# Kernel optimization log

Hardware: AMD Instinct MI355X
Metric: run time of the kernel (lower is better)

The kernel has to match this reference:

```python
import jax, jax.numpy as jnp
import numpy as np

# heavy-atom counts minus 1 (the residue_len) for the 20 standard amino acids
# GLY ALA SER CYS THR VAL PRO LEU ILE ASN ASP MET GLN GLU LYS HIS PHE ARG TYR TRP
NATOMS = np.array([4,5,6,6,7,7,7,8,8,8,8,8,9,9,9,10,11,11,12,14], dtype=np.int64)
NTYPES = 20
MAXA = int(NATOMS.max())  # 14
B, R, VDIM, NLIN = 128, 512, 256, 3


def setup_inputs() -> dict:
    rng = np.random.default_rng(0)
    type_ids = rng.integers(0, NTYPES, size=R)                     # metadata.seq as type ids
    natoms = NATOMS[type_ids]                                      # per-residue atom count
    residue_indices = np.concatenate([[0], np.cumsum(natoms)[:-1]])  # start atom of each residue
    n_atoms = int(natoms.sum())

    key = jax.random.key(0)
    k1, k2, k3 = jax.random.split(key, 3)
    x = jax.random.normal(k1, (B, n_atoms, 3), dtype=jnp.float32)

    # per-type first-layer weight, zero-padded beyond each type's natom so the
    # padded gathered atoms contribute exactly zero (identical math to slicing)
    pad_mask = (np.arange(MAXA)[None, :] < NATOMS[:, None]).astype(np.float32)  # (T, A)
    W0 = jax.random.normal(k2, (NTYPES, VDIM, MAXA), dtype=jnp.float32)
    W0 = W0 * (1.0 / np.sqrt(MAXA)) * jnp.asarray(pad_mask)[:, None, :]
    Wh = jax.random.normal(k3, (NTYPES, NLIN - 1, VDIM, VDIM), dtype=jnp.float32) * (1.0 / np.sqrt(VDIM))

    return {
        "x": x,
        "W0": W0,
        "Wh": Wh,
        "type_ids": jnp.asarray(type_ids, dtype=jnp.int64),
        "residue_indices": jnp.asarray(residue_indices, dtype=jnp.int64),
    }


def reference(x, W0, Wh, type_ids, residue_indices):
    """x:(B, atoms, 3) -> pos_ca:(B, R, 3), x_v:(B, R, VDIM, 3)"""
    n_atoms = x.shape[1]
    # gather each residue's atom window, padded to MAXA (clip keeps indices in
    # range; padded entries are killed by the zero-padded W0 columns)
    atom_idx = jnp.clip(residue_indices[:, None] + jnp.arange(MAXA)[None, :], 0, n_atoms - 1)  # (R, A)
    gathered = x[:, atom_idx]                               # (B, R, A, 3)
    root = x[:, residue_indices + 1]                        # (B, R, 3)  -- CA atom (x[:,1] of each slice)
    delta = gathered - root[:, :, None, :]                  # subtract root

    h = jnp.einsum('rva,brac->brvc', W0[type_ids], delta)   # per-type VecLinear(natom -> vdim)
    for l in range(NLIN - 1):                               # per-type VecLinear(vdim -> vdim)
        h = jnp.einsum('rvu,bruc->brvc', Wh[type_ids, l], h)

    pos_ca = root                                            # x[:, residue_indices + 1]
    return pos_ca, h
```

## Files before the change

### kernel.cpp

```cpp
#include <hip/hip_runtime.h>

namespace {
constexpr int NB = 128;
constexpr int NR = 512;
constexpr int ND = 256;
constexpr int NA = 14;

using short8 = __attribute__((ext_vector_type(8))) short;
using f32x4  = __attribute__((ext_vector_type(4))) float;

constexpr size_t WH_US  = (size_t)40 * 16 * 8 * 64 * 8;
constexpr size_t W0_OFF = WH_US;
constexpr size_t W0_US  = (size_t)20 * 16 * 64 * 8;
constexpr size_t RMAP_BYTE_OFF = (WH_US + W0_US) * 2;
constexpr size_t WS_NEEDED = RMAP_BYTE_OFF + NR * sizeof(int);

__device__ __forceinline__ unsigned short f2bf(float f) {
    unsigned int u = __float_as_uint(f);
    u = (u + 0x7FFFu + ((u >> 16) & 1u)) >> 16;
    return (unsigned short)u;
}
__device__ __forceinline__ int vswz(int v) { return v ^ (((v >> 5) & 3) << 3); }
}

__global__ void conv_wh(const float* __restrict__ Wh, unsigned short* __restrict__ ws) {
    int g = blockIdx.x * 256 + threadIdx.x;
    if (g >= 40 * 16 * 8 * 64) return;
    const int lane = g & 63, kt = (g >> 6) & 7, mt = (g >> 9) & 15, tl = g >> 13;
    const int v = mt * 16 + (lane & 15);
    const int u0 = kt * 32 + (lane >> 4) * 8;
    const float* src = Wh + ((size_t)tl * ND + v) * ND + u0;
    unsigned short o[8];
#pragma unroll
    for (int j = 0; j < 8; ++j) o[j] = f2bf(src[j]);
    uint4 pk;
    pk.x = o[0] | ((unsigned)o[1] << 16); pk.y = o[2] | ((unsigned)o[3] << 16);
    pk.z = o[4] | ((unsigned)o[5] << 16); pk.w = o[6] | ((unsigned)o[7] << 16);
    *reinterpret_cast<uint4*>(ws + (size_t)g * 8) = pk;
}

__global__ void conv_w0(const float* __restrict__ W0, unsigned short* __restrict__ ws) {
    int g = blockIdx.x * 256 + threadIdx.x;
    if (g >= 20 * 16 * 64) return;
    const int lane = g & 63, mt = (g >> 6) & 15, t = g >> 10;
    const int v = mt * 16 + (lane & 15);
    const int a0 = (lane >> 4) * 8;
    unsigned short o[8];
#pragma unroll
    for (int j = 0; j < 8; ++j) {
        const int a = a0 + j;
        o[j] = (a < NA) ? f2bf(W0[((size_t)t * ND + v) * NA + a]) : (unsigned short)0;
    }
    uint4 pk;
    pk.x = o[0] | ((unsigned)o[1] << 16); pk.y = o[2] | ((unsigned)o[3] << 16);
    pk.z = o[4] | ((unsigned)o[5] << 16); pk.w = o[6] | ((unsigned)o[7] << 16);
    *reinterpret_cast<uint4*>(ws + W0_OFF + (size_t)g * 8) = pk;
}

__global__ void build_rmap(const int* __restrict__ type_ids, int* __restrict__ rmap) {
    __shared__ int tl[NR];
    const int tid = threadIdx.x;
    tl[tid] = type_ids[tid];
    __syncthreads();
    const int myt = tl[tid];
    int pos = 0;
    for (int j = 0; j < NR; ++j) {
        const int tj = tl[j];
        pos += (tj < myt) || (tj == myt && j < tid);
    }
    rmap[pos] = tid;
}

__global__ __launch_bounds__(512, 6) void residues_mfma(
    const float* __restrict__ x, const unsigned short* __restrict__ wsw,
    const int* __restrict__ rmap, const int* __restrict__ type_ids,
    const int* __restrict__ res_idx, float* __restrict__ out, int n_atoms)
{
    const int tid = threadIdx.x, lane = tid & 63, w = tid >> 6;
    const int xcd = blockIdx.x & 7, j = blockIdx.x >> 3;
    const int r = rmap[xcd * 64 + (j >> 3)];
    const int b0 = (j & 7) * 16;
    const int ri = res_idx[r], t = type_ids[r];

    __shared__ __align__(16) unsigned short HT[48 * 264];
    __shared__ __align__(16) float fstc[24 * 260];
    unsigned short* dltT = HT;

    const unsigned short* w0b = wsw + W0_OFF + (size_t)t * (16 * 64 * 8);
    short8 a0[2];
#pragma unroll
    for (int mi = 0; mi < 2; ++mi)
        a0[mi] = *reinterpret_cast<const short8*>(w0b + (((w * 2 + mi) * 64) + lane) * 8);

    {
        const int bl = tid >> 5, k = tid & 31;
        const float* xb = x + (size_t)(b0 + bl) * n_atoms * 3;
        if (k < 16) {
            int atom = ri + k; if (atom > n_atoms - 1) atom = n_atoms - 1;
            const float* src  = xb + (size_t)atom * 3;
            const float* root = xb + (size_t)(ri + 1) * 3;
#pragma unroll
            for (int c = 0; c < 3; ++c)
                dltT[(bl * 3 + c) * 40 + k] = f2bf(src[c] - root[c]);
            if (k == 1) {
#pragma unroll
                for (int c = 0; c < 3; ++c)
                    out[((size_t)(b0 + bl) * NR + r) * 3 + c] = root[c];
            }
        } else {
#pragma unroll
            for (int c = 0; c < 3; ++c)
                dltT[(bl * 3 + c) * 40 + k] = 0;
        }
    }
    __syncthreads();

    f32x4 acc[2][3];
#pragma unroll
    for (int mi = 0; mi < 2; ++mi)
#pragma unroll
        for (int ni = 0; ni < 3; ++ni) acc[mi][ni] = f32x4{0.f, 0.f, 0.f, 0.f};

    {
        short8 bf[3];
#pragma unroll
        for (int ni = 0; ni < 3; ++ni)
            bf[ni] = *reinterpret_cast<const short8*>(&dltT[(ni * 16 + (lane & 15)) * 40 + (lane >> 4) * 8]);
#pragma unroll
        for (int mi = 0; mi < 2; ++mi)
#pragma unroll
            for (int ni = 0; ni < 3; ++ni)
                acc[mi][ni] = __builtin_amdgcn_mfma_f32_16x16x32_bf16(a0[mi], bf[ni], acc[mi][ni], 0, 0, 0);
    }
    __syncthreads();

#pragma unroll 1
    for (int l = 0; l < 2; ++l) {
#pragma unroll
        for (int mi = 0; mi < 2; ++mi)
#pragma unroll
            for (int ni = 0; ni < 3; ++ni) {
                const int v0 = w * 32 + mi * 16 + (lane >> 4) * 4;
                const int n  = ni * 16 + (lane & 15);
                const unsigned lo = (unsigned)f2bf(acc[mi][ni][0]) | ((unsigned)f2bf(acc[mi][ni][1]) << 16);
                const unsigned hi = (unsigned)f2bf(acc[mi][ni][2]) | ((unsigned)f2bf(acc[mi][ni][3]) << 16);
                *reinterpret_cast<uint2*>(&HT[n * 264 + v0]) = make_uint2(lo, hi);
            }
        __syncthreads();

#pragma unroll
        for (int mi = 0; mi < 2; ++mi)
#pragma unroll
            for (int ni = 0; ni < 3; ++ni) acc[mi][ni] = f32x4{0.f, 0.f, 0.f, 0.f};

        const unsigned short* wl = wsw + (size_t)(t * 2 + l) * (16 * 8 * 64 * 8);
#pragma unroll 1
        for (int kt = 0; kt < 8; ++kt) {
            short8 a[2], bf[3];
#pragma unroll
            for (int mi = 0; mi < 2; ++mi)
                a[mi] = *reinterpret_cast<const short8*>(wl + ((((w * 2 + mi) * 8 + kt) * 64) + lane) * 8);
#pragma unroll
            for (int ni = 0; ni < 3; ++ni)
                bf[ni] = *reinterpret_cast<const short8*>(&HT[(ni * 16 + (lane & 15)) * 264 + kt * 32 + (lane >> 4) * 8]);
#pragma unroll
            for (int mi = 0; mi < 2; ++mi)
#pragma unroll
                for (int ni = 0; ni < 3; ++ni)
                    acc[mi][ni] = __builtin_amdgcn_mfma_f32_16x16x32_bf16(a[mi], bf[ni], acc[mi][ni], 0, 0, 0);
        }
        if (l == 0) __syncthreads();
    }

    float* outh = out + (size_t)NB * NR * 3;
#pragma unroll 1
    for (int q = 0; q < 2; ++q) {
#pragma unroll
        for (int mi = 0; mi < 2; ++mi)
#pragma unroll
            for (int ni = 0; ni < 3; ++ni) {
                const int n = ni * 16 + (lane & 15);
                const int nloc = n - 24 * q;
                if (nloc >= 0 && nloc < 24) {
                    const int vb = w * 32 + mi * 16 + (lane >> 4) * 4;
                    *reinterpret_cast<f32x4*>(&fstc[nloc * 260 + vswz(vb)]) = acc[mi][ni];
                }
            }
        __syncthreads();
        {
            const size_t obase = ((size_t)(b0 + 8 * q + w) * NR + r) * (ND * 3);
#pragma unroll
            for (int i = 0; i < 3; ++i) {
                const int f0 = (lane + 64 * i) * 4;
                int v = f0 / 3;
                int c = f0 - v * 3;
                f32x4 o;
#pragma unroll
                for (int e = 0; e < 4; ++e) {
                    o[e] = fstc[(w * 3 + c) * 260 + vswz(v)];
                    ++c; if (c == 3) { c = 0; ++v; }
                }
                __builtin_nontemporal_store(o,
                    reinterpret_cast<f32x4*>(&outh[obase + f0]));
            }
        }
        if (q == 0) __syncthreads();
    }
}

__global__ __launch_bounds__(256, 3) void residues_fused_fb(
    const float* __restrict__ x, const float* __restrict__ W0,
    const float* __restrict__ Wh, const int* __restrict__ type_ids,
    const int* __restrict__ res_idx, float* __restrict__ out, int n_atoms)
{
    const int tid = threadIdx.x;
    const int r = blockIdx.x >> 4;
    const int b0 = (blockIdx.x & 15) * 8;
    const int ri = res_idx[r], t = type_ids[r];
    __shared__ float dlt[NA][24];
    __shared__ float hA[ND][24];
    __shared__ float hB[ND][24];
    for (int idx = tid; idx < 8 * NA * 3; idx += 256) {
        const int bb = idx / (NA * 3), rem = idx % (NA * 3);
        const int a = rem / 3, c = rem % 3, b = b0 + bb;
        int ca = ri + a; if (ca > n_atoms - 1) ca = n_atoms - 1;
        const float root = x[((size_t)b * n_atoms + (ri + 1)) * 3 + c];
        dlt[a][bb * 3 + c] = x[((size_t)b * n_atoms + ca) * 3 + c] - root;
        if (a == 0) out[((size_t)b * NR + r) * 3 + c] = root;
    }
    __syncthreads();
    {
        const float* w0row = W0 + ((size_t)t * ND + tid) * NA;
        float acc[24];
#pragma unroll
        for (int n = 0; n < 24; ++n) acc[n] = 0.f;
#pragma unroll
        for (int a = 0; a < NA; ++a) {
            const float wv = w0row[a];
#pragma unroll
            for (int n = 0; n < 24; ++n) acc[n] += wv * dlt[a][n];
        }
#pragma unroll
        for (int n = 0; n < 24; ++n) hA[tid][n] = acc[n];
    }
    __syncthreads();
    const float* whbase = Wh + (size_t)t * 2 * ND * ND;
#pragma unroll
    for (int l = 0; l < 2; ++l) {
        const float* wrow = whbase + ((size_t)l * ND + tid) * ND;
        const float (*hin)[24] = (l == 0) ? hA : hB;
        float (*hout)[24]      = (l == 0) ? hB : hA;
        float acc[24];
#pragma unroll
        for (int n = 0; n < 24; ++n) acc[n] = 0.f;
        for (int u = 0; u < ND; ++u) {
            const float wv = wrow[u];
#pragma unroll
            for (int n = 0; n < 24; ++n) acc[n] += wv * hin[u][n];
        }
#pragma unroll
        for (int n = 0; n < 24; ++n) hout[tid][n] = acc[n];
        __syncthreads();
    }
    float* outh = out + (size_t)NB * NR * 3;
#pragma unroll
    for (int bb = 0; bb < 8; ++bb) {
        const size_t base = ((size_t)((b0 + bb) * NR + r)) * (ND * 3);
#pragma unroll
        for (int it = 0; it < 3; ++it) {
            const int g = it * 256 + tid;
            outh[base + g] = hA[g / 3][bb * 3 + g % 3];
        }
    }
}

extern "C" void kernel_launch(void* const* d_in, const int* in_sizes, int n_in,
                              void* d_out, int out_size, void* d_ws, size_t ws_size,
                              hipStream_t stream) {
    const float* x        = (const float*)d_in[0];
    const float* W0       = (const float*)d_in[1];
    const float* Wh       = (const float*)d_in[2];
    const int*   type_ids = (const int*)d_in[3];
    const int*   res_idx  = (const int*)d_in[4];
    float* out = (float*)d_out;
    const int n_atoms = in_sizes[0] / (NB * 3);

    if (ws_size >= WS_NEEDED) {
        unsigned short* wsw = (unsigned short*)d_ws;
        int* rmap = (int*)((char*)d_ws + RMAP_BYTE_OFF);
        conv_wh<<<(40 * 16 * 8 * 64 + 255) / 256, 256, 0, stream>>>(Wh, wsw);
        conv_w0<<<(20 * 16 * 64 + 255) / 256, 256, 0, stream>>>(W0, wsw);
        build_rmap<<<1, NR, 0, stream>>>(type_ids, rmap);
        residues_mfma<<<NR * 8, 512, 0, stream>>>(x, wsw, rmap, type_ids, res_idx, out, n_atoms);
    } else {
        residues_fused_fb<<<NR * 16, 256, 0, stream>>>(x, W0, Wh, type_ids, res_idx, out, n_atoms);
    }
}
```

Before: 101.7 us.

## Process two batch chunks per block with double-buffered H and prefetched atom deltas

Result: no change. 100.4 us (-1.3%).

```diff
diff --git a/kernel.cpp b/kernel.cpp
--- a/kernel.cpp
+++ b/kernel.cpp
@@ -71,20 +71,23 @@
     rmap[pos] = tid;
 }
 
-__global__ __launch_bounds__(512, 6) void residues_mfma(
+__global__ __launch_bounds__(512, 4) void residues_mfma(
     const float* __restrict__ x, const unsigned short* __restrict__ wsw,
     const int* __restrict__ rmap, const int* __restrict__ type_ids,
     const int* __restrict__ res_idx, float* __restrict__ out, int n_atoms)
 {
     const int tid = threadIdx.x, lane = tid & 63, w = tid >> 6;
     const int xcd = blockIdx.x & 7, j = blockIdx.x >> 3;
-    const int r = rmap[xcd * 64 + (j >> 3)];
-    const int b0 = (j & 7) * 16;
+    const int r = rmap[xcd * 64 + (j >> 2)];
+    const int b00 = (j & 3) * 32;
     const int ri = res_idx[r], t = type_ids[r];
 
-    __shared__ __align__(16) unsigned short HT[48 * 264];
-    __shared__ __align__(16) float fstc[24 * 260];
-    unsigned short* dltT = HT;
+    __shared__ __align__(16) unsigned short dlt[2][48 * 40];
+    __shared__ __align__(16) unsigned short HT2[2 * 48 * 264];
+    unsigned short* HTa = HT2;
+    unsigned short* HTb = HT2 + 48 * 264;
+    float* eps = reinterpret_cast<float*>(HT2);
+    float* outh = out + (size_t)NB * NR * 3;
 
     const unsigned short* w0b = wsw + W0_OFF + (size_t)t * (16 * 64 * 8);
     short8 a0[2];
@@ -94,48 +97,50 @@
 
     {
         const int bl = tid >> 5, k = tid & 31;
-        const float* xb = x + (size_t)(b0 + bl) * n_atoms * 3;
+        const float* xb = x + (size_t)(b00 + bl) * n_atoms * 3;
         if (k < 16) {
             int atom = ri + k; if (atom > n_atoms - 1) atom = n_atoms - 1;
             const float* src  = xb + (size_t)atom * 3;
             const float* root = xb + (size_t)(ri + 1) * 3;
 #pragma unroll
             for (int c = 0; c < 3; ++c)
-                dltT[(bl * 3 + c) * 40 + k] = f2bf(src[c] - root[c]);
+                dlt[0][(bl * 3 + c) * 40 + k] = f2bf(src[c] - root[c]);
             if (k == 1) {
 #pragma unroll
                 for (int c = 0; c < 3; ++c)
-                    out[((size_t)(b0 + bl) * NR + r) * 3 + c] = root[c];
+                    out[((size_t)(b00 + bl) * NR + r) * 3 + c] = root[c];
             }
         } else {
 #pragma unroll
             for (int c = 0; c < 3; ++c)
-                dltT[(bl * 3 + c) * 40 + k] = 0;
+                dlt[0][(bl * 3 + c) * 40 + k] = 0;
         }
     }
     __syncthreads();
 
-    f32x4 acc[2][3];
-#pragma unroll
-    for (int mi = 0; mi < 2; ++mi)
-#pragma unroll
-        for (int ni = 0; ni < 3; ++ni) acc[mi][ni] = f32x4{0.f, 0.f, 0.f, 0.f};
-
-    {
-        short8 bf[3];
-#pragma unroll
-        for (int ni = 0; ni < 3; ++ni)
-            bf[ni] = *reinterpret_cast<const short8*>(&dltT[(ni * 16 + (lane & 15)) * 40 + (lane >> 4) * 8]);
-#pragma unroll
-        for (int mi = 0; mi < 2; ++mi)
+    float s0 = 0, s1 = 0, s2 = 0, r0v = 0, r1v = 0, r2v = 0;
+
+#pragma unroll
+    for (int u = 0; u < 2; ++u) {
+        const int b0 = b00 + u * 16;
+
+        f32x4 acc[2][3];
+#pragma unroll
+        for (int mi = 0; mi < 2; ++mi)
+#pragma unroll
+            for (int ni = 0; ni < 3; ++ni) acc[mi][ni] = f32x4{0.f, 0.f, 0.f, 0.f};
+
+        {
+            short8 bf[3];
 #pragma unroll
             for (int ni = 0; ni < 3; ++ni)
-                acc[mi][ni] = __builtin_amdgcn_mfma_f32_16x16x32_bf16(a0[mi], bf[ni], acc[mi][ni], 0, 0, 0);
-    }
-    __syncthreads();
-
-#pragma unroll 1
-    for (int l = 0; l < 2; ++l) {
+                bf[ni] = *reinterpret_cast<const short8*>(&dlt[u][(ni * 16 + (lane & 15)) * 40 + (lane >> 4) * 8]);
+#pragma unroll
+            for (int mi = 0; mi < 2; ++mi)
+#pragma unroll
+                for (int ni = 0; ni < 3; ++ni)
+                    acc[mi][ni] = __builtin_amdgcn_mfma_f32_16x16x32_bf16(a0[mi], bf[ni], acc[mi][ni], 0, 0, 0);
+        }
 #pragma unroll
         for (int mi = 0; mi < 2; ++mi)
 #pragma unroll
@@ -144,51 +149,110 @@
                 const int n  = ni * 16 + (lane & 15);
                 const unsigned lo = (unsigned)f2bf(acc[mi][ni][0]) | ((unsigned)f2bf(acc[mi][ni][1]) << 16);
                 const unsigned hi = (unsigned)f2bf(acc[mi][ni][2]) | ((unsigned)f2bf(acc[mi][ni][3]) << 16);
-                *reinterpret_cast<uint2*>(&HT[n * 264 + v0]) = make_uint2(lo, hi);
-            }
+                *reinterpret_cast<uint2*>(&HTa[n * 264 + v0]) = make_uint2(lo, hi);
+            }
+        if (u == 0) {
+            const int bl = tid >> 5, k = tid & 31;
+            if (k < 16) {
+                int atom = ri + k; if (atom > n_atoms - 1) atom = n_atoms - 1;
+                const float* xb1 = x + (size_t)(b00 + 16 + bl) * n_atoms * 3;
+                const float* sp = xb1 + (size_t)atom * 3;
+                const float* rp = xb1 + (size_t)(ri + 1) * 3;
+                s0 = sp[0]; s1 = sp[1]; s2 = sp[2];
+                r0v = rp[0]; r1v = rp[1]; r2v = rp[2];
+            }
+        }
         __syncthreads();
 
 #pragma unroll
         for (int mi = 0; mi < 2; ++mi)
 #pragma unroll
             for (int ni = 0; ni < 3; ++ni) acc[mi][ni] = f32x4{0.f, 0.f, 0.f, 0.f};
-
-        const unsigned short* wl = wsw + (size_t)(t * 2 + l) * (16 * 8 * 64 * 8);
+        {
+            const unsigned short* wl = wsw + (size_t)(t * 2 + 0) * (16 * 8 * 64 * 8);
 #pragma unroll 1
-        for (int kt = 0; kt < 8; ++kt) {
-            short8 a[2], bf[3];
-#pragma unroll
-            for (int mi = 0; mi < 2; ++mi)
-                a[mi] = *reinterpret_cast<const short8*>(wl + ((((w * 2 + mi) * 8 + kt) * 64) + lane) * 8);
-#pragma unroll
-            for (int ni = 0; ni < 3; ++ni)
-                bf[ni] = *reinterpret_cast<const short8*>(&HT[(ni * 16 + (lane & 15)) * 264 + kt * 32 + (lane >> 4) * 8]);
-#pragma unroll
-            for (int mi = 0; mi < 2; ++mi)
+            for (int kt = 0; kt < 8; ++kt) {
+                short8 a[2], bf[3];
+#pragma unroll
+                for (int mi = 0; mi < 2; ++mi)
+                    a[mi] = *reinterpret_cast<const short8*>(wl + ((((w * 2 + mi) * 8 + kt) * 64) + lane) * 8);
 #pragma unroll
                 for (int ni = 0; ni < 3; ++ni)
-                    acc[mi][ni] = __builtin_amdgcn_mfma_f32_16x16x32_bf16(a[mi], bf[ni], acc[mi][ni], 0, 0, 0);
-        }
-        if (l == 0) __syncthreads();
-    }
-
-    float* outh = out + (size_t)NB * NR * 3;
+                    bf[ni] = *reinterpret_cast<const short8*>(&HTa[(ni * 16 + (lane & 15)) * 264 + kt * 32 + (lane >> 4) * 8]);
+#pragma unroll
+                for (int mi = 0; mi < 2; ++mi)
+#pragma unroll
+                    for (int ni = 0; ni < 3; ++ni)
+                        acc[mi][ni] = __builtin_amdgcn_mfma_f32_16x16x32_bf16(a[mi], bf[ni], acc[mi][ni], 0, 0, 0);
+            }
+        }
+#pragma unroll
+        for (int mi = 0; mi < 2; ++mi)
+#pragma unroll
+            for (int ni = 0; ni < 3; ++ni) {
+                const int v0 = w * 32 + mi * 16 + (lane >> 4) * 4;
+                const int n  = ni * 16 + (lane & 15);
+                const unsigned lo = (unsigned)f2bf(acc[mi][ni][0]) | ((unsigned)f2bf(acc[mi][ni][1]) << 16);
+                const unsigned hi = (unsigned)f2bf(acc[mi][ni][2]) | ((unsigned)f2bf(acc[mi][ni][3]) << 16);
+                *reinterpret_cast<uint2*>(&HTb[n * 264 + v0]) = make_uint2(lo, hi);
+            }
+        __syncthreads();
+
+#pragma unroll
+        for (int mi = 0; mi < 2; ++mi)
+#pragma unroll
+            for (int ni = 0; ni < 3; ++ni) acc[mi][ni] = f32x4{0.f, 0.f, 0.f, 0.f};
+        {
+            const unsigned short* wl = wsw + (size_t)(t * 2 + 1) * (16 * 8 * 64 * 8);
 #pragma unroll 1
-    for (int q = 0; q < 2; ++q) {
+            for (int kt = 0; kt < 8; ++kt) {
+                short8 a[2], bf[3];
+#pragma unroll
+                for (int mi = 0; mi < 2; ++mi)
+                    a[mi] = *reinterpret_cast<const short8*>(wl + ((((w * 2 + mi) * 8 + kt) * 64) + lane) * 8);
+#pragma unroll
+                for (int ni = 0; ni < 3; ++ni)
+                    bf[ni] = *reinterpret_cast<const short8*>(&HTb[(ni * 16 + (lane & 15)) * 264 + kt * 32 + (lane >> 4) * 8]);
+#pragma unroll
+                for (int mi = 0; mi < 2; ++mi)
+#pragma unroll
+                    for (int ni = 0; ni < 3; ++ni)
+                        acc[mi][ni] = __builtin_amdgcn_mfma_f32_16x16x32_bf16(a[mi], bf[ni], acc[mi][ni], 0, 0, 0);
+            }
+        }
+        if (u == 0) {
+            const int bl = tid >> 5, k = tid & 31;
+            if (k < 16) {
+                dlt[1][(bl * 3 + 0) * 40 + k] = f2bf(s0 - r0v);
+                dlt[1][(bl * 3 + 1) * 40 + k] = f2bf(s1 - r1v);
+                dlt[1][(bl * 3 + 2) * 40 + k] = f2bf(s2 - r2v);
+                if (k == 1) {
+                    out[((size_t)(b00 + 16 + bl) * NR + r) * 3 + 0] = r0v;
+                    out[((size_t)(b00 + 16 + bl) * NR + r) * 3 + 1] = r1v;
+                    out[((size_t)(b00 + 16 + bl) * NR + r) * 3 + 2] = r2v;
+                }
+            } else {
+#pragma unroll
+                for (int c = 0; c < 3; ++c)
+                    dlt[1][(bl * 3 + c) * 40 + k] = 0;
+            }
+        }
+        __syncthreads();
+
 #pragma unroll
         for (int mi = 0; mi < 2; ++mi)
 #pragma unroll
             for (int ni = 0; ni < 3; ++ni) {
-                const int n = ni * 16 + (lane & 15);
-                const int nloc = n - 24 * q;
-                if (nloc >= 0 && nloc < 24) {
-                    const int vb = w * 32 + mi * 16 + (lane >> 4) * 4;
-                    *reinterpret_cast<f32x4*>(&fstc[nloc * 260 + vswz(vb)]) = acc[mi][ni];
-                }
-            }
-        __syncthreads();
-        {
-            const size_t obase = ((size_t)(b0 + 8 * q + w) * NR + r) * (ND * 3);
+                const int n  = ni * 16 + (lane & 15);
+                const int vb = w * 32 + mi * 16 + (lane >> 4) * 4;
+                *reinterpret_cast<f32x4*>(&eps[n * 260 + vswz(vb)]) = acc[mi][ni];
+            }
+        __syncthreads();
+
+#pragma unroll
+        for (int h = 0; h < 2; ++h) {
+            const int wb = w + 8 * h;
+            const size_t ob = ((size_t)(b0 + wb) * NR + r) * (ND * 3);
 #pragma unroll
             for (int i = 0; i < 3; ++i) {
                 const int f0 = (lane + 64 * i) * 4;
@@ -197,14 +261,14 @@
                 f32x4 o;
 #pragma unroll
                 for (int e = 0; e < 4; ++e) {
-                    o[e] = fstc[(w * 3 + c) * 260 + vswz(v)];
+                    o[e] = eps[(wb * 3 + c) * 260 + vswz(v)];
                     ++c; if (c == 3) { c = 0; ++v; }
                 }
                 __builtin_nontemporal_store(o,
-                    reinterpret_cast<f32x4*>(&outh[obase + f0]));
-            }
-        }
-        if (q == 0) __syncthreads();
+                    reinterpret_cast<f32x4*>(&outh[ob + f0]));
+            }
+        }
+        if (u == 0) __syncthreads();
     }
 }
 
@@ -291,7 +355,7 @@
         conv_wh<<<(40 * 16 * 8 * 64 + 255) / 256, 256, 0, stream>>>(Wh, wsw);
         conv_w0<<<(20 * 16 * 64 + 255) / 256, 256, 0, stream>>>(W0, wsw);
         build_rmap<<<1, NR, 0, stream>>>(type_ids, rmap);
-        residues_mfma<<<NR * 8, 512, 0, stream>>>(x, wsw, rmap, type_ids, res_idx, out, n_atoms);
+        residues_mfma<<<NR * 4, 512, 0, stream>>>(x, wsw, rmap, type_ids, res_idx, out, n_atoms);
     } else {
         residues_fused_fb<<<NR * 16, 256, 0, stream>>>(x, W0, Wh, type_ids, res_idx, out, n_atoms);
     }
```

## Fold per-type weight chain into a single matrix before applying to residues

Applied to the files above, without the earlier changes.

Result: slower. 111.1 us (+9.3%).

```diff
diff --git a/kernel.cpp b/kernel.cpp
--- a/kernel.cpp
+++ b/kernel.cpp
@@ -5,92 +5,131 @@
 constexpr int NR = 512;
 constexpr int ND = 256;
 constexpr int NA = 14;
+constexpr int NT = 20;
 
 using short8 = __attribute__((ext_vector_type(8))) short;
 using f32x4  = __attribute__((ext_vector_type(4))) float;
 
-constexpr size_t WH_US  = (size_t)40 * 16 * 8 * 64 * 8;
-constexpr size_t W0_OFF = WH_US;
-constexpr size_t W0_US  = (size_t)20 * 16 * 64 * 8;
-constexpr size_t RMAP_BYTE_OFF = (WH_US + W0_US) * 2;
-constexpr size_t WS_NEEDED = RMAP_BYTE_OFF + NR * sizeof(int);
+constexpr size_t M_US      = (size_t)NT * 16 * 64 * 8;
+constexpr size_t WS_NEEDED = M_US * 2;
 
 __device__ __forceinline__ unsigned short f2bf(float f) {
     unsigned int u = __float_as_uint(f);
     u = (u + 0x7FFFu + ((u >> 16) & 1u)) >> 16;
     return (unsigned short)u;
 }
+__device__ __forceinline__ short8 cvt8(const float* p) {
+    short8 r;
+#pragma unroll
+    for (int j = 0; j < 8; ++j) r[j] = (short)f2bf(p[j]);
+    return r;
+}
 __device__ __forceinline__ int vswz(int v) { return v ^ (((v >> 5) & 3) << 3); }
 }
 
-__global__ void conv_wh(const float* __restrict__ Wh, unsigned short* __restrict__ ws) {
-    int g = blockIdx.x * 256 + threadIdx.x;
-    if (g >= 40 * 16 * 8 * 64) return;
-    const int lane = g & 63, kt = (g >> 6) & 7, mt = (g >> 9) & 15, tl = g >> 13;
-    const int v = mt * 16 + (lane & 15);
-    const int u0 = kt * 32 + (lane >> 4) * 8;
-    const float* src = Wh + ((size_t)tl * ND + v) * ND + u0;
-    unsigned short o[8];
-#pragma unroll
-    for (int j = 0; j < 8; ++j) o[j] = f2bf(src[j]);
-    uint4 pk;
-    pk.x = o[0] | ((unsigned)o[1] << 16); pk.y = o[2] | ((unsigned)o[3] << 16);
-    pk.z = o[4] | ((unsigned)o[5] << 16); pk.w = o[6] | ((unsigned)o[7] << 16);
-    *reinterpret_cast<uint4*>(ws + (size_t)g * 8) = pk;
-}
-
-__global__ void conv_w0(const float* __restrict__ W0, unsigned short* __restrict__ ws) {
-    int g = blockIdx.x * 256 + threadIdx.x;
-    if (g >= 20 * 16 * 64) return;
-    const int lane = g & 63, mt = (g >> 6) & 15, t = g >> 10;
-    const int v = mt * 16 + (lane & 15);
-    const int a0 = (lane >> 4) * 8;
-    unsigned short o[8];
-#pragma unroll
-    for (int j = 0; j < 8; ++j) {
-        const int a = a0 + j;
-        o[j] = (a < NA) ? f2bf(W0[((size_t)t * ND + v) * NA + a]) : (unsigned short)0;
-    }
-    uint4 pk;
-    pk.x = o[0] | ((unsigned)o[1] << 16); pk.y = o[2] | ((unsigned)o[3] << 16);
-    pk.z = o[4] | ((unsigned)o[5] << 16); pk.w = o[6] | ((unsigned)o[7] << 16);
-    *reinterpret_cast<uint4*>(ws + W0_OFF + (size_t)g * 8) = pk;
-}
-
-__global__ void build_rmap(const int* __restrict__ type_ids, int* __restrict__ rmap) {
-    __shared__ int tl[NR];
-    const int tid = threadIdx.x;
-    tl[tid] = type_ids[tid];
-    __syncthreads();
-    const int myt = tl[tid];
-    int pos = 0;
-    for (int j = 0; j < NR; ++j) {
-        const int tj = tl[j];
-        pos += (tj < myt) || (tj == myt && j < tid);
-    }
-    rmap[pos] = tid;
-}
-
-__global__ __launch_bounds__(512, 6) void residues_mfma(
-    const float* __restrict__ x, const unsigned short* __restrict__ wsw,
-    const int* __restrict__ rmap, const int* __restrict__ type_ids,
-    const int* __restrict__ res_idx, float* __restrict__ out, int n_atoms)
+__global__ __launch_bounds__(256) void fold_M(
+    const float* __restrict__ W0, const float* __restrict__ Wh,
+    unsigned short* __restrict__ wsM)
+{
+    const int t = blockIdx.x, tid = threadIdx.x, lane = tid & 63, w = tid >> 6;
+    __shared__ __align__(16) unsigned short T1T[16 * 264];
+    __shared__ __align__(16) unsigned short MT[16 * 264];
+
+    short8 bw0[8];
+    {
+        const int a = lane & 15;
+#pragma unroll
+        for (int kt = 0; kt < 8; ++kt) {
+            unsigned short o[8];
+#pragma unroll
+            for (int j = 0; j < 8; ++j) {
+                const int u = kt * 32 + (lane >> 4) * 8 + j;
+                o[j] = (a < NA) ? f2bf(W0[((size_t)t * ND + u) * NA + a]) : (unsigned short)0;
+            }
+            short8 v;
+#pragma unroll
+            for (int j = 0; j < 8; ++j) v[j] = (short)o[j];
+            bw0[kt] = v;
+        }
+    }
+
+    f32x4 acc[4];
+#pragma unroll
+    for (int mi = 0; mi < 4; ++mi) acc[mi] = f32x4{0.f, 0.f, 0.f, 0.f};
+#pragma unroll 1
+    for (int kt = 0; kt < 8; ++kt) {
+#pragma unroll
+        for (int mi = 0; mi < 4; ++mi) {
+            const int v = (w * 4 + mi) * 16 + (lane & 15);
+            const float* src = Wh + (((size_t)(t * 2 + 0) * ND + v) * ND) + kt * 32 + (lane >> 4) * 8;
+            acc[mi] = __builtin_amdgcn_mfma_f32_16x16x32_bf16(cvt8(src), bw0[kt], acc[mi], 0, 0, 0);
+        }
+    }
+#pragma unroll
+    for (int mi = 0; mi < 4; ++mi) {
+        const int v0 = (w * 4 + mi) * 16 + (lane >> 4) * 4;
+        const int a  = lane & 15;
+        const unsigned lo = (unsigned)f2bf(acc[mi][0]) | ((unsigned)f2bf(acc[mi][1]) << 16);
+        const unsigned hi = (unsigned)f2bf(acc[mi][2]) | ((unsigned)f2bf(acc[mi][3]) << 16);
+        *reinterpret_cast<uint2*>(&T1T[a * 264 + v0]) = make_uint2(lo, hi);
+    }
+    __syncthreads();
+
+#pragma unroll
+    for (int mi = 0; mi < 4; ++mi) acc[mi] = f32x4{0.f, 0.f, 0.f, 0.f};
+#pragma unroll 1
+    for (int kt = 0; kt < 8; ++kt) {
+        const short8 bf = *reinterpret_cast<const short8*>(&T1T[(lane & 15) * 264 + kt * 32 + (lane >> 4) * 8]);
+#pragma unroll
+        for (int mi = 0; mi < 4; ++mi) {
+            const int v = (w * 4 + mi) * 16 + (lane & 15);
+            const float* src = Wh + (((size_t)(t * 2 + 1) * ND + v) * ND) + kt * 32 + (lane >> 4) * 8;
+            acc[mi] = __builtin_amdgcn_mfma_f32_16x16x32_bf16(cvt8(src), bf, acc[mi], 0, 0, 0);
+        }
+    }
+#pragma unroll
+    for (int mi = 0; mi < 4; ++mi) {
+        const int v0 = (w * 4 + mi) * 16 + (lane >> 4) * 4;
+        const int a  = lane & 15;
+        const unsigned lo = (unsigned)f2bf(acc[mi][0]) | ((unsigned)f2bf(acc[mi][1]) << 16);
+        const unsigned hi = (unsigned)f2bf(acc[mi][2]) | ((unsigned)f2bf(acc[mi][3]) << 16);
+        *reinterpret_cast<uint2*>(&MT[a * 264 + v0]) = make_uint2(lo, hi);
+    }
+    __syncthreads();
+
+    for (int g = tid; g < 16 * 64; g += 256) {
+        const int mt = g >> 6, l2 = g & 63;
+        const int v = mt * 16 + (l2 & 15);
+        unsigned short o[8];
+#pragma unroll
+        for (int j = 0; j < 8; ++j) {
+            const int k = (l2 >> 4) * 8 + j;
+            o[j] = (k < NA) ? MT[k * 264 + v] : (unsigned short)0;
+        }
+        uint4 pk;
+        pk.x = o[0] | ((unsigned)o[1] << 16); pk.y = o[2] | ((unsigned)o[3] << 16);
+        pk.z = o[4] | ((unsigned)o[5] << 16); pk.w = o[6] | ((unsigned)o[7] << 16);
+        *reinterpret_cast<uint4*>(wsM + ((size_t)(t * 16 + mt) * 64 + l2) * 8) = pk;
+    }
+}
+
+__global__ __launch_bounds__(512, 4) void residues_main(
+    const float* __restrict__ x, const unsigned short* __restrict__ wsM,
+    const int* __restrict__ type_ids, const int* __restrict__ res_idx,
+    float* __restrict__ out, int n_atoms)
 {
     const int tid = threadIdx.x, lane = tid & 63, w = tid >> 6;
-    const int xcd = blockIdx.x & 7, j = blockIdx.x >> 3;
-    const int r = rmap[xcd * 64 + (j >> 3)];
-    const int b0 = (j & 7) * 16;
+    const int r = blockIdx.x >> 3;
+    const int b0 = (blockIdx.x & 7) * 16;
     const int ri = res_idx[r], t = type_ids[r];
 
-    __shared__ __align__(16) unsigned short HT[48 * 264];
+    __shared__ __align__(16) unsigned short dltT[48 * 40];
     __shared__ __align__(16) float fstc[24 * 260];
-    unsigned short* dltT = HT;
-
-    const unsigned short* w0b = wsw + W0_OFF + (size_t)t * (16 * 64 * 8);
-    short8 a0[2];
+
+    short8 aM[2];
 #pragma unroll
     for (int mi = 0; mi < 2; ++mi)
-        a0[mi] = *reinterpret_cast<const short8*>(w0b + (((w * 2 + mi) * 64) + lane) * 8);
+        aM[mi] = *reinterpret_cast<const short8*>(wsM + ((size_t)(t * 16 + w * 2 + mi) * 64 + lane) * 8);
 
     {
         const int bl = tid >> 5, k = tid & 31;
@@ -120,7 +159,6 @@
     for (int mi = 0; mi < 2; ++mi)
 #pragma unroll
         for (int ni = 0; ni < 3; ++ni) acc[mi][ni] = f32x4{0.f, 0.f, 0.f, 0.f};
-
     {
         short8 bf[3];
 #pragma unroll
@@ -130,46 +168,7 @@
         for (int mi = 0; mi < 2; ++mi)
 #pragma unroll
             for (int ni = 0; ni < 3; ++ni)
-                acc[mi][ni] = __builtin_amdgcn_mfma_f32_16x16x32_bf16(a0[mi], bf[ni], acc[mi][ni], 0, 0, 0);
-    }
-    __syncthreads();
-
-#pragma unroll 1
-    for (int l = 0; l < 2; ++l) {
-#pragma unroll
-        for (int mi = 0; mi < 2; ++mi)
-#pragma unroll
-            for (int ni = 0; ni < 3; ++ni) {
-                const int v0 = w * 32 + mi * 16 + (lane >> 4) * 4;
-                const int n  = ni * 16 + (lane & 15);
-                const unsigned lo = (unsigned)f2bf(acc[mi][ni][0]) | ((unsigned)f2bf(acc[mi][ni][1]) << 16);
-                const unsigned hi = (unsigned)f2bf(acc[mi][ni][2]) | ((unsigned)f2bf(acc[mi][ni][3]) << 16);
-                *reinterpret_cast<uint2*>(&HT[n * 264 + v0]) = make_uint2(lo, hi);
-            }
-        __syncthreads();
-
-#pragma unroll
-        for (int mi = 0; mi < 2; ++mi)
-#pragma unroll
-            for (int ni = 0; ni < 3; ++ni) acc[mi][ni] = f32x4{0.f, 0.f, 0.f, 0.f};
-
-        const unsigned short* wl = wsw + (size_t)(t * 2 + l) * (16 * 8 * 64 * 8);
-#pragma unroll 1
-        for (int kt = 0; kt < 8; ++kt) {
-            short8 a[2], bf[3];
-#pragma unroll
-            for (int mi = 0; mi < 2; ++mi)
-                a[mi] = *reinterpret_cast<const short8*>(wl + ((((w * 2 + mi) * 8 + kt) * 64) + lane) * 8);
-#pragma unroll
-            for (int ni = 0; ni < 3; ++ni)
-                bf[ni] = *reinterpret_cast<const short8*>(&HT[(ni * 16 + (lane & 15)) * 264 + kt * 32 + (lane >> 4) * 8]);
-#pragma unroll
-            for (int mi = 0; mi < 2; ++mi)
-#pragma unroll
-                for (int ni = 0; ni < 3; ++ni)
-                    acc[mi][ni] = __builtin_amdgcn_mfma_f32_16x16x32_bf16(a[mi], bf[ni], acc[mi][ni], 0, 0, 0);
-        }
-        if (l == 0) __syncthreads();
+                acc[mi][ni] = __builtin_amdgcn_mfma_f32_16x16x32_bf16(aM[mi], bf[ni], acc[mi][ni], 0, 0, 0);
     }
 
     float* outh = out + (size_t)NB * NR * 3;
@@ -286,12 +285,9 @@
     const int n_atoms = in_sizes[0] / (NB * 3);
 
     if (ws_size >= WS_NEEDED) {
-        unsigned short* wsw = (unsigned short*)d_ws;
-        int* rmap = (int*)((char*)d_ws + RMAP_BYTE_OFF);
-        conv_wh<<<(40 * 16 * 8 * 64 + 255) / 256, 256, 0, stream>>>(Wh, wsw);
-        conv_w0<<<(20 * 16 * 64 + 255) / 256, 256, 0, stream>>>(W0, wsw);
-        build_rmap<<<1, NR, 0, stream>>>(type_ids, rmap);
-        residues_mfma<<<NR * 8, 512, 0, stream>>>(x, wsw, rmap, type_ids, res_idx, out, n_atoms);
+        unsigned short* wsM = (unsigned short*)d_ws;
+        fold_M<<<NT, 256, 0, stream>>>(W0, Wh, wsM);
+        residues_main<<<NR * 8, 512, 0, stream>>>(x, wsM, type_ids, res_idx, out, n_atoms);
     } else {
         residues_fused_fb<<<NR * 16, 256, 0, stream>>>(x, W0, Wh, type_ids, res_idx, out, n_atoms);
     }
```
